# Kernel tuning notes

Hardware: AMD Instinct MI355X
Metric: run time of the kernel (lower is better)

Reference implementation:

```python
import jax, jax.numpy as jnp
import numpy as np


def setup_inputs() -> dict:
    key = jax.random.key(0)
    k_x, k_w, k_b = jax.random.split(key, 3)
    B, Cin, H, W = 32, 256, 56, 56
    Cout, KH, KW = 256, 3, 3
    x = jax.random.normal(k_x, (B, Cin, H, W), dtype=jnp.float32)
    fp_weight = jax.random.normal(k_w, (Cout, Cin, KH, KW), dtype=jnp.float32)
    # binary quantization, conv_mode='input_ch': per-output-channel scale
    scaling_factors = jnp.mean(jnp.abs(fp_weight), axis=(1, 2, 3), keepdims=True)  # [Cout,1,1,1]
    quant_weights = jnp.sign(fp_weight)  # values in {-1,0,1}
    bias = jax.random.normal(k_b, (Cout,), dtype=jnp.float32)
    return {"x": x, "scaling_factors": scaling_factors,
            "quant_weights": quant_weights, "bias": bias}


def reference(x, scaling_factors, quant_weights, bias):
    # Dequantize: per-out-channel scale times sign weights
    new_weights = scaling_factors * quant_weights  # [Cout,Cin,3,3]
    out = jax.lax.conv_general_dilated(
        x, new_weights,
        window_strides=(1, 1),
        padding=((1, 1), (1, 1)),
        dimension_numbers=("NCHW", "OIHW", "NCHW"),
    )
    return out + bias[None, :, None, None]
```

## Files before the change

### kernel.cpp

```cpp
#include <hip/hip_runtime.h>

using half8   = __attribute__((ext_vector_type(8))) _Float16;
using floatx4 = __attribute__((ext_vector_type(4))) float;
using floatx2 = __attribute__((ext_vector_type(2))) float;
using short8  = __attribute__((ext_vector_type(8))) short;

#define XT_ROW_ELEMS 2560
#define XT_ROW_BYTES 5120
#define XT_OFF ((size_t)2 << 20)
#define XT_BYTES ((size_t)256 * 58 * XT_ROW_BYTES)

__device__ __forceinline__ void dma16(const void* g, void* l) {
  __builtin_amdgcn_global_load_lds(
      (const __attribute__((address_space(1))) void*)g,
      (__attribute__((address_space(3))) void*)l, 16, 0, 0);
}

__global__ __launch_bounds__(256) void prep_kernel(
    const float* __restrict__ x, const float* __restrict__ qw,
    _Float16* __restrict__ wre, _Float16* __restrict__ xt)
{
  const int bid = blockIdx.x;
  const int t = threadIdx.x;
  if (bid >= 14848) {
    int idx = (bid - 14848) * 256 + t;
    int c = idx & 255, co = (idx >> 8) & 255, s = idx >> 16;
    wre[idx] = (_Float16)qw[(co * 256 + c) * 9 + s];
    return;
  }
  __shared__ _Float16 lt[32 * 57];
  const int hh = bid % 58;
  const int bc = bid / 58;
  const int cc = bc & 7, b = bc >> 3;
  _Float16* dst = xt + ((size_t)bc * 58 + hh) * XT_ROW_ELEMS;
  const bool interior = (hh >= 1) && (hh <= 56);
  if (interior) {
    const int c = t >> 3, j = t & 7;
    const float* src = x + (((size_t)(b * 256 + cc * 32 + c)) * 56 + (hh - 1)) * 56 + j * 7;
#pragma unroll
    for (int i = 0; i < 7; ++i) lt[c * 57 + j * 7 + i] = (_Float16)src[i];
  }
  __syncthreads();
  for (int ch = t; ch < 320; ch += 256) {
    int pos = ch / 5, sl = ch - pos * 5;
    short8 v = {0, 0, 0, 0, 0, 0, 0, 0};
    if (interior && sl < 4 && pos >= 1 && pos <= 56) {
      int w = pos - 1;
#pragma unroll
      for (int i = 0; i < 8; ++i)
        v[i] = __builtin_bit_cast(short, lt[(sl * 8 + i) * 57 + w]);
    }
    *reinterpret_cast<short8*>(dst + ch * 8) = v;
  }
}

__global__ __launch_bounds__(256, 2) void binconv_v4(
    const float* __restrict__ scale, const float* __restrict__ bias,
    const _Float16* __restrict__ wre, const _Float16* __restrict__ xt,
    float* __restrict__ out)
{
  __shared__ _Float16 xs[2 * 4 * 64 * 40];

  const int tid  = threadIdx.x;
  const int nb   = blockIdx.x;
  const int b    = nb / 28;
  const int h0   = (nb % 28) * 2;
  const int wave = tid >> 6;
  const int lane = tid & 63;
  const int nl   = lane & 15;
  const int quad = lane >> 4;
  const int co_wave = wave * 64;

  int bbase[7];
#pragma unroll
  for (int j = 0; j < 7; ++j) {
    int n = j * 16 + nl;
    int r = (n >= 56) ? 1 : 0;
    int w = n - r * 56;
    bbase[j] = (r * 64 + w) * 80 + quad * 16;
  }

  const _Float16* aptr[4];
#pragma unroll
  for (int mi = 0; mi < 4; ++mi)
    aptr[mi] = wre + (co_wave + mi * 16 + nl) * 256 + quad * 8;

  floatx4 acc[4][7];
#pragma unroll
  for (int mi = 0; mi < 4; ++mi)
#pragma unroll
    for (int j = 0; j < 7; ++j)
      acc[mi][j] = (floatx4){0.f, 0.f, 0.f, 0.f};

  const char* xsrc = (const char*)(xt + ((size_t)(b * 8) * 58 + h0) * XT_ROW_ELEMS);
  const int wlane = wave * XT_ROW_BYTES + lane * 16;
  const int wldso = wave * XT_ROW_BYTES;

#pragma unroll
  for (int i = 0; i < 5; ++i)
    dma16(xsrc + wlane + i * 1024, (char*)xs + wldso + i * 1024);

  half8 acur[4], anxt[4];
#pragma unroll
  for (int mi = 0; mi < 4; ++mi)
    acur[mi] = *reinterpret_cast<const half8*>(aptr[mi]);

  int bufoff = 0;
  for (int cc = 0; cc < 8; ++cc) {
    __syncthreads();
    if (cc < 7) {
      const char* srcn = xsrc + (size_t)(cc + 1) * (58 * XT_ROW_BYTES);
#pragma unroll
      for (int i = 0; i < 5; ++i)
        dma16(srcn + wlane + i * 1024,
              (char*)xs + (bufoff ^ 20480) + wldso + i * 1024);
    }
    const int c0 = cc * 32;
    const char* xb = (const char*)xs + bufoff;

    half8 bcur[7], bnxt[7];
#pragma unroll
    for (int j = 0; j < 7; ++j)
      bcur[j] = *reinterpret_cast<const half8*>(xb + bbase[j]);

#pragma unroll
    for (int s = 0; s < 9; ++s) {
      if (s < 8) {
        const int kh1 = (s + 1) / 3, kw1 = (s + 1) - kh1 * 3;
        const int soff1 = (kh1 * 64 + kw1) * 80;
#pragma unroll
        for (int j = 0; j < 7; ++j)
          bnxt[j] = *reinterpret_cast<const half8*>(xb + bbase[j] + soff1);
      }
      if (cc < 7 || s < 8) {
        const int s1 = (s < 8) ? s + 1 : 0;
        const int c1 = (s < 8) ? c0 : c0 + 32;
#pragma unroll
        for (int mi = 0; mi < 4; ++mi)
          anxt[mi] = *reinterpret_cast<const half8*>(aptr[mi] + s1 * 65536 + c1);
      }
      __builtin_amdgcn_s_setprio(1);
#pragma unroll
      for (int j = 0; j < 7; ++j)
#pragma unroll
        for (int mi = 0; mi < 4; ++mi)
          acc[mi][j] = __builtin_amdgcn_mfma_f32_16x16x32_f16(acur[mi], bcur[j], acc[mi][j], 0, 0, 0);
      __builtin_amdgcn_s_setprio(0);
#pragma unroll
      for (int mi = 0; mi < 4; ++mi) acur[mi] = anxt[mi];
#pragma unroll
      for (int j = 0; j < 7; ++j) bcur[j] = bnxt[j];
    }
    bufoff ^= 20480;
  }

#pragma unroll
  for (int mi = 0; mi < 4; ++mi) {
#pragma unroll
    for (int reg = 0; reg < 4; ++reg) {
      int co = co_wave + mi * 16 + quad * 4 + reg;
      float s_ = scale[co];
      float bi = bias[co];
#pragma unroll
      for (int j = 0; j < 7; ++j) {
        int n = j * 16 + nl;
        int r = (n >= 56) ? 1 : 0;
        int w = n - r * 56;
        out[(((size_t)b * 256 + co) * 56 + (h0 + r)) * 56 + w] =
            acc[mi][j][reg] * s_ + bi;
      }
    }
  }
}

__global__ void repack_weights(const float* __restrict__ qw,
                               _Float16* __restrict__ wre, int n) {
  int t = blockIdx.x * 256 + threadIdx.x;
  if (t >= n) return;
  int c = t & 255, co = (t >> 8) & 255, s = t >> 16;
  wre[t] = (_Float16)qw[(co * 256 + c) * 9 + s];
}

__global__ __launch_bounds__(512, 4) void binconv_fused(
    const float* __restrict__ x, const float* __restrict__ scale,
    const float* __restrict__ bias, const _Float16* __restrict__ wre,
    float* __restrict__ out)
{
  __shared__ _Float16 xs[2 * 4 * 64 * 40];
  const int tid  = threadIdx.x;
  const int nb   = blockIdx.x;
  const int b    = nb / 28;
  const int h0   = (nb % 28) * 2;
  const int wave = tid >> 6;
  const int lane = tid & 63;
  const int nl   = lane & 15;
  const int quad = lane >> 4;
  const int co_wave = wave * 32;
  {
    short8 z = {0, 0, 0, 0, 0, 0, 0, 0};
    short8* xs8 = reinterpret_cast<short8*>(xs);
#pragma unroll
    for (int i = 0; i < 5; ++i) xs8[tid + i * 512] = z;
  }
  const int r     = wave >> 1;
  const int chalf = wave & 1;
  const int sc    = lane & 15;
  const int q     = lane >> 4;
  const int ch    = chalf * 16 + sc;
  const int w0    = q * 14;
  const int h     = h0 + r - 1;
  const bool hok  = (h >= 0) && (h < 56);
  const float* xc = x + (((size_t)b * 256 + ch) * 56 + (hok ? h : 0)) * 56 + w0;
  _Float16* const wrow = xs + r * 2560 + ch;
  floatx2 va[7];
  int bbase[7];
#pragma unroll
  for (int j = 0; j < 7; ++j) {
    int n = j * 16 + nl;
    int rr = (n >= 56) ? 1 : 0;
    int w = n - rr * 56;
    bbase[j] = (rr * 64 + w) * 80 + quad * 16;
  }
  const _Float16* aptr[2];
#pragma unroll
  for (int mi = 0; mi < 2; ++mi)
    aptr[mi] = wre + (co_wave + mi * 16 + nl) * 256 + quad * 8;
  floatx4 acc[2][7];
#pragma unroll
  for (int mi = 0; mi < 2; ++mi)
#pragma unroll
    for (int j = 0; j < 7; ++j)
      acc[mi][j] = (floatx4){0.f, 0.f, 0.f, 0.f};
  __syncthreads();
  if (hok) {
#pragma unroll
    for (int i = 0; i < 7; ++i)
      va[i] = *reinterpret_cast<const floatx2*>(xc + 2 * i);
#pragma unroll
    for (int i = 0; i < 7; ++i) {
      wrow[(w0 + 2 * i + 1) * 40] = (_Float16)va[i][0];
      wrow[(w0 + 2 * i + 2) * 40] = (_Float16)va[i][1];
    }
  }
  int bufe = 0;
  for (int cc = 0; cc < 8; ++cc) {
    __syncthreads();
    if (cc < 7 && hok) {
      const float* A = xc + (size_t)(cc + 1) * 100352;
#pragma unroll
      for (int i = 0; i < 7; ++i)
        va[i] = *reinterpret_cast<const floatx2*>(A + 2 * i);
    }
    const int c0 = cc * 32;
    const char* xb = reinterpret_cast<const char*>(xs) + bufe * 2;
#pragma unroll
    for (int s = 0; s < 9; ++s) {
      const int kh = s / 3, kw = s - kh * 3;
      half8 a[2];
#pragma unroll
      for (int mi = 0; mi < 2; ++mi)
        a[mi] = *reinterpret_cast<const half8*>(aptr[mi] + s * 65536 + c0);
      const int soff = (kh * 64 + kw) * 80;
#pragma unroll
      for (int j = 0; j < 7; ++j) {
        half8 bf = *reinterpret_cast<const half8*>(xb + bbase[j] + soff);
#pragma unroll
        for (int mi = 0; mi < 2; ++mi)
          acc[mi][j] = __builtin_amdgcn_mfma_f32_16x16x32_f16(a[mi], bf, acc[mi][j], 0, 0, 0);
      }
    }
    if (cc < 7 && hok) {
      _Float16* d = wrow + (bufe ^ 10240);
#pragma unroll
      for (int i = 0; i < 7; ++i) {
        d[(w0 + 2 * i + 1) * 40] = (_Float16)va[i][0];
        d[(w0 + 2 * i + 2) * 40] = (_Float16)va[i][1];
      }
    }
    bufe ^= 10240;
  }
#pragma unroll
  for (int mi = 0; mi < 2; ++mi) {
#pragma unroll
    for (int reg = 0; reg < 4; ++reg) {
      int co = co_wave + mi * 16 + quad * 4 + reg;
      float s_ = scale[co];
      float bi = bias[co];
#pragma unroll
      for (int j = 0; j < 7; ++j) {
        int n = j * 16 + nl;
        int rr = (n >= 56) ? 1 : 0;
        int w = n - rr * 56;
        out[(((size_t)b * 256 + co) * 56 + (h0 + rr)) * 56 + w] =
            acc[mi][j][reg] * s_ + bi;
      }
    }
  }
}

extern "C" void kernel_launch(void* const* d_in, const int* in_sizes, int n_in,
                              void* d_out, int out_size, void* d_ws, size_t ws_size,
                              hipStream_t stream) {
  const float* x     = (const float*)d_in[0];
  const float* scale = (const float*)d_in[1];
  const float* qw    = (const float*)d_in[2];
  const float* bias  = (const float*)d_in[3];
  float* out = (float*)d_out;

  _Float16* wre = (_Float16*)d_ws;

  if (ws_size >= XT_OFF + XT_BYTES) {
    _Float16* xt = (_Float16*)((char*)d_ws + XT_OFF);
    prep_kernel<<<17152, 256, 0, stream>>>(x, qw, wre, xt);
    binconv_v4<<<896, 256, 0, stream>>>(scale, bias, wre, xt, out);
  } else {
    repack_weights<<<2304, 256, 0, stream>>>(qw, wre, 9 * 256 * 256);
    binconv_fused<<<896, 512, 0, stream>>>(x, scale, bias, wre, out);
  }
}
```

Baseline: 329.6 us.

## Triple-buffer LDS input tiles with explicit waitcnt and drop register prefetch

Moves the input-tile staging from double to triple buffering, issuing DMA two channel chunks ahead and synchronising with explicit vmcnt waits and raw s_barrier in place of __syncthreads. It also removes the register-level prefetching of A and B fragments: weights and LDS operands are now loaded right before their MFMAs, with B fragments loaded one at a time per column tile. This is meant to hide global-to-LDS latency better and lower register pressure. In exchange it uses 50% more LDS per block, which may limit occupancy, and it exposes LDS and global load latency inside the MFMA loop.

```diff
diff --git a/kernel.cpp b/kernel.cpp
--- a/kernel.cpp
+++ b/kernel.cpp
@@ -54,12 +54,12 @@
   }
 }
 
-__global__ __launch_bounds__(256, 2) void binconv_v4(
+__global__ __launch_bounds__(256, 2) void binconv_v5(
     const float* __restrict__ scale, const float* __restrict__ bias,
     const _Float16* __restrict__ wre, const _Float16* __restrict__ xt,
     float* __restrict__ out)
 {
-  __shared__ _Float16 xs[2 * 4 * 64 * 40];
+  __shared__ _Float16 xs[3 * 4 * 64 * 40];
 
   const int tid  = threadIdx.x;
   const int nb   = blockIdx.x;
@@ -99,59 +99,45 @@
 #pragma unroll
   for (int i = 0; i < 5; ++i)
     dma16(xsrc + wlane + i * 1024, (char*)xs + wldso + i * 1024);
-
-  half8 acur[4], anxt[4];
-#pragma unroll
-  for (int mi = 0; mi < 4; ++mi)
-    acur[mi] = *reinterpret_cast<const half8*>(aptr[mi]);
-
-  int bufoff = 0;
+#pragma unroll
+  for (int i = 0; i < 5; ++i)
+    dma16(xsrc + (58 * XT_ROW_BYTES) + wlane + i * 1024,
+          (char*)xs + 20480 + wldso + i * 1024);
+
+  int cur = 0, nxt = 20480, nx2 = 40960;
   for (int cc = 0; cc < 8; ++cc) {
-    __syncthreads();
-    if (cc < 7) {
-      const char* srcn = xsrc + (size_t)(cc + 1) * (58 * XT_ROW_BYTES);
+    if (cc < 7) asm volatile("s_waitcnt vmcnt(5) lgkmcnt(0)" ::: "memory");
+    else        asm volatile("s_waitcnt vmcnt(0) lgkmcnt(0)" ::: "memory");
+    __builtin_amdgcn_sched_barrier(0);
+    __builtin_amdgcn_s_barrier();
+    __builtin_amdgcn_sched_barrier(0);
+    if (cc < 6) {
+      const char* srcn = xsrc + (size_t)(cc + 2) * (58 * XT_ROW_BYTES);
 #pragma unroll
       for (int i = 0; i < 5; ++i)
-        dma16(srcn + wlane + i * 1024,
-              (char*)xs + (bufoff ^ 20480) + wldso + i * 1024);
+        dma16(srcn + wlane + i * 1024, (char*)xs + nx2 + wldso + i * 1024);
     }
     const int c0 = cc * 32;
-    const char* xb = (const char*)xs + bufoff;
-
-    half8 bcur[7], bnxt[7];
-#pragma unroll
-    for (int j = 0; j < 7; ++j)
-      bcur[j] = *reinterpret_cast<const half8*>(xb + bbase[j]);
-
+    const char* xb = (const char*)xs + cur;
+    __builtin_amdgcn_s_setprio(1);
 #pragma unroll
     for (int s = 0; s < 9; ++s) {
-      if (s < 8) {
-        const int kh1 = (s + 1) / 3, kw1 = (s + 1) - kh1 * 3;
-        const int soff1 = (kh1 * 64 + kw1) * 80;
-#pragma unroll
-        for (int j = 0; j < 7; ++j)
-          bnxt[j] = *reinterpret_cast<const half8*>(xb + bbase[j] + soff1);
-      }
-      if (cc < 7 || s < 8) {
-        const int s1 = (s < 8) ? s + 1 : 0;
-        const int c1 = (s < 8) ? c0 : c0 + 32;
+      const int kh = s / 3, kw = s - kh * 3;
+      half8 a[4];
+#pragma unroll
+      for (int mi = 0; mi < 4; ++mi)
+        a[mi] = *reinterpret_cast<const half8*>(aptr[mi] + s * 65536 + c0);
+      const int soff = (kh * 64 + kw) * 80;
+#pragma unroll
+      for (int j = 0; j < 7; ++j) {
+        half8 bf = *reinterpret_cast<const half8*>(xb + bbase[j] + soff);
 #pragma unroll
         for (int mi = 0; mi < 4; ++mi)
-          anxt[mi] = *reinterpret_cast<const half8*>(aptr[mi] + s1 * 65536 + c1);
-      }
-      __builtin_amdgcn_s_setprio(1);
-#pragma unroll
-      for (int j = 0; j < 7; ++j)
-#pragma unroll
-        for (int mi = 0; mi < 4; ++mi)
-          acc[mi][j] = __builtin_amdgcn_mfma_f32_16x16x32_f16(acur[mi], bcur[j], acc[mi][j], 0, 0, 0);
-      __builtin_amdgcn_s_setprio(0);
-#pragma unroll
-      for (int mi = 0; mi < 4; ++mi) acur[mi] = anxt[mi];
-#pragma unroll
-      for (int j = 0; j < 7; ++j) bcur[j] = bnxt[j];
-    }
-    bufoff ^= 20480;
+          acc[mi][j] = __builtin_amdgcn_mfma_f32_16x16x32_f16(a[mi], bf, acc[mi][j], 0, 0, 0);
+      }
+    }
+    __builtin_amdgcn_s_setprio(0);
+    int t_ = cur; cur = nxt; nxt = nx2; nx2 = t_;
   }
 
 #pragma unroll
@@ -312,7 +298,7 @@
   if (ws_size >= XT_OFF + XT_BYTES) {
     _Float16* xt = (_Float16*)((char*)d_ws + XT_OFF);
     prep_kernel<<<17152, 256, 0, stream>>>(x, qw, wre, xt);
-    binconv_v4<<<896, 256, 0, stream>>>(scale, bias, wre, xt, out);
+    binconv_v5<<<896, 256, 0, stream>>>(scale, bias, wre, xt, out);
   } else {
     repack_weights<<<2304, 256, 0, stream>>>(qw, wre, 9 * 256 * 256);
     binconv_fused<<<896, 512, 0, stream>>>(x, scale, bias, wre, out);
```

After: 335.6 us. About the same (+1.8%).
